# Performance work log

Hardware: AMD Instinct MI355X
Metric: run time of the kernel (lower is better)

The kernel has to match this reference:

```python
import jax, jax.numpy as jnp
import numpy as np

N_NODES = 50000
N_EDGES = 800000
D_IN = 128
D_HID = 128
BN_EPS = 1e-5


def _sage_mean(h, src, dst, w_self, w_neigh, b):
    # DGL SAGEConv('mean'): out = h @ W_self + mean_{neighbors}(h_src) @ W_neigh + bias
    msg = h[src]                                               # [E, D] gather
    ssum = jax.ops.segment_sum(msg, dst, num_segments=N_NODES)  # [N, D]
    deg = jax.ops.segment_sum(jnp.ones((src.shape[0],), h.dtype), dst,
                              num_segments=N_NODES)            # [N]
    mean = ssum / jnp.maximum(deg, 1.0)[:, None]
    return h @ w_self + mean @ w_neigh + b


def _bn_relu(h, gamma, beta):
    # BatchNorm1d with batch statistics (training-mode math), then ReLU.
    m = jnp.mean(h, axis=0)
    v = jnp.mean(jnp.square(h - m), axis=0)  # biased variance, as torch uses for normalization
    hn = (h - m) * jax.lax.rsqrt(v + BN_EPS) * gamma + beta
    return jax.nn.relu(hn)


def setup_inputs() -> dict:
    key = jax.random.key(0)
    ks = jax.random.split(key, 16)
    x = jax.random.normal(ks[0], (N_NODES, D_IN), dtype=jnp.float32)
    src = jax.random.randint(ks[1], (N_EDGES,), 0, N_NODES, dtype=jnp.int32)
    dst = jax.random.randint(ks[2], (N_EDGES,), 0, N_NODES, dtype=jnp.int32)
    s0 = 1.0 / np.sqrt(D_IN)
    s1 = 1.0 / np.sqrt(D_HID)
    inp = {
        'x': x, 'src': src, 'dst': dst,
        'W_self0': jax.random.uniform(ks[3], (D_IN, D_HID), jnp.float32, -s0, s0),
        'W_neigh0': jax.random.uniform(ks[4], (D_IN, D_HID), jnp.float32, -s0, s0),
        'b0': jnp.zeros((D_HID,), jnp.float32),
        'W_self1': jax.random.uniform(ks[5], (D_HID, D_HID), jnp.float32, -s1, s1),
        'W_neigh1': jax.random.uniform(ks[6], (D_HID, D_HID), jnp.float32, -s1, s1),
        'b1': jnp.zeros((D_HID,), jnp.float32),
        'W_self2': jax.random.uniform(ks[7], (D_HID, D_HID), jnp.float32, -s1, s1),
        'W_neigh2': jax.random.uniform(ks[8], (D_HID, D_HID), jnp.float32, -s1, s1),
        'b2': jnp.zeros((D_HID,), jnp.float32),
        'gamma0': jnp.ones((D_HID,), jnp.float32),
        'beta0': jnp.zeros((D_HID,), jnp.float32),
        'gamma1': jnp.ones((D_HID,), jnp.float32),
        'beta1': jnp.zeros((D_HID,), jnp.float32),
    }
    return inp


def reference(x, src, dst,
              W_self0, W_neigh0, b0,
              W_self1, W_neigh1, b1,
              W_self2, W_neigh2, b2,
              gamma0, beta0, gamma1, beta1):
    h = _sage_mean(x, src, dst, W_self0, W_neigh0, b0)
    h = _bn_relu(h, gamma0, beta0)  # dropout is identity in eval mode
    h = _sage_mean(h, src, dst, W_self1, W_neigh1, b1)
    h = _bn_relu(h, gamma1, beta1)
    h = _sage_mean(h, src, dst, W_self2, W_neigh2, b2)
    return h
```

## Files before the change

### kernel.cpp

```cpp
#include <hip/hip_runtime.h>

#define N_NODES 50000
#define N_EDGES 800000
#define D 128
#define BN_EPS 1e-5f

#define NBUCK 391
#define BSHIFT 7
#define S1_BLOCKS 256
#define EPB 3125
#define CVT_BLOCKS 6250
#define PACK_BLOCKS 384
#define NREP 16
#define NSLICE 8
#define SSHIFT 13
#define BN_BLOCKS 512

typedef __attribute__((ext_vector_type(8))) short bf16x8;
typedef __attribute__((ext_vector_type(4))) float f32x4;
typedef __attribute__((ext_vector_type(2))) float f32x2;

__device__ inline unsigned short f2bf(float f) {
    unsigned int u = __float_as_uint(f);
    u = (u + 0x7FFF + ((u >> 16) & 1)) >> 16;
    return (unsigned short)u;
}

__device__ inline float bf2f(unsigned short b) {
    return __uint_as_float(((unsigned)b) << 16);
}

__device__ __forceinline__ void acc_plain(f32x2* a, uint4 v) {
    unsigned w[4] = {v.x, v.y, v.z, v.w};
#pragma unroll
    for (int p = 0; p < 4; p++) {
        f32x2 f;
        f.x = __uint_as_float(w[p] << 16);
        f.y = __uint_as_float(w[p] & 0xffff0000u);
        a[p] += f;
    }
}


__global__ void fused_prep(const float* __restrict__ x, unsigned short* __restrict__ x16,
                           const int* __restrict__ dst, int* __restrict__ hist,
                           const float* __restrict__ Ws0, const float* __restrict__ Wn0,
                           const float* __restrict__ Ws1, const float* __restrict__ Wn1,
                           const float* __restrict__ Ws2, const float* __restrict__ Wn2,
                           unsigned short* __restrict__ Wf, float* __restrict__ statsg) {
    __shared__ int lh[NBUCK];
    const int bid = blockIdx.x, t = threadIdx.x;

    if (bid < CVT_BLOCKS) {
        int idx = bid * 256 + t;
        float4 v = ((const float4*)x)[idx];
        ushort4 o;
        o.x = f2bf(v.x); o.y = f2bf(v.y); o.z = f2bf(v.z); o.w = f2bf(v.w);
        ((ushort4*)x16)[idx] = o;
    } else if (bid < CVT_BLOCKS + S1_BLOCKS) {
        int blk = bid - CVT_BLOCKS;
        for (int i = t; i < NBUCK; i += 256) lh[i] = 0;
        __syncthreads();
        int e0 = blk * EPB;
        for (int i = 0; i < 13; i++) {
            int k = t + i * 256;
            if (k < EPB) atomicAdd(&lh[dst[e0 + k] >> BSHIFT], 1);
        }
        __syncthreads();
        for (int i = t; i < NBUCK; i += 256) hist[blk * NBUCK + i] = lh[i];
    } else {
        if (bid == CVT_BLOCKS + S1_BLOCKS) {
            for (int i = t; i < 2 * NREP * 256; i += 256) statsg[i] = 0.f;
        }
        int idx = (bid - (CVT_BLOCKS + S1_BLOCKS)) * 256 + t;
        if (idx < 3 * 32768) {
            int layer = idx >> 15;
            int rem = idx & 32767;
            int kt = rem >> 12;
            int nt = (rem >> 9) & 7;
            int lane = (rem >> 3) & 63;
            int j = rem & 7;
            int k = kt * 32 + (lane >> 4) * 8 + j;
            int n = nt * 16 + (lane & 15);
            const float* Wsrc;
            if (layer == 0) Wsrc = (k < 128) ? Ws0 : Wn0;
            else if (layer == 1) Wsrc = (k < 128) ? Ws1 : Wn1;
            else Wsrc = (k < 128) ? Ws2 : Wn2;
            Wf[idx] = f2bf(Wsrc[(k & 127) * D + n]);
        }
    }
}


__global__ void s2a(int* __restrict__ hist, int* __restrict__ bucketTotal) {
    __shared__ int s[S1_BLOCKS];
    int b = blockIdx.x, t = threadIdx.x;
    int v = hist[t * NBUCK + b];
    s[t] = v;
    __syncthreads();
    for (int off = 1; off < S1_BLOCKS; off <<= 1) {
        int x = (t >= off) ? s[t - off] : 0;
        __syncthreads();
        s[t] += x;
        __syncthreads();
    }
    hist[t * NBUCK + b] = s[t] - v;
    if (t == S1_BLOCKS - 1) bucketTotal[b] = s[t];
}


__global__ void s3_scatter(const int* __restrict__ src, const int* __restrict__ dst,
                           const int* __restrict__ hist, const int* __restrict__ bucketTotal,
                           int* __restrict__ bucketStart, unsigned int* __restrict__ rec) {
    __shared__ int sc[512];
    __shared__ int base[NBUCK];
    int blk = blockIdx.x, t = threadIdx.x;
    int i1 = t + 256;
    int v0 = (t < NBUCK) ? bucketTotal[t] : 0;
    int v1 = (i1 < NBUCK) ? bucketTotal[i1] : 0;
    sc[t] = v0; sc[i1] = v1;
    __syncthreads();
    for (int off = 1; off < 512; off <<= 1) {
        int x0 = (t >= off) ? sc[t - off] : 0;
        int x1 = (i1 >= off) ? sc[i1 - off] : 0;
        __syncthreads();
        sc[t] += x0; sc[i1] += x1;
        __syncthreads();
    }
    if (t < NBUCK)  base[t]  = (sc[t] - v0)  + hist[blk * NBUCK + t];
    if (i1 < NBUCK) base[i1] = (sc[i1] - v1) + hist[blk * NBUCK + i1];
    if (blk == 0) {
        if (t < NBUCK)  bucketStart[t]  = sc[t] - v0;
        if (i1 < NBUCK) bucketStart[i1] = sc[i1] - v1;
        if (t == 0) bucketStart[NBUCK] = N_EDGES;
    }
    __syncthreads();
    int e0 = blk * EPB;
    for (int i = 0; i < 13; i++) {
        int k = t + i * 256;
        if (k < EPB) {
            int e = e0 + k;
            int d = dst[e];
            int p = atomicAdd(&base[d >> BSHIFT], 1);
            rec[p] = ((unsigned)(d & 127) << 16) | (unsigned)src[e];
        }
    }
}


__global__ void s4_build(const unsigned int* __restrict__ rec, const int* __restrict__ bucketStart,
                         unsigned short* __restrict__ csr, int* __restrict__ degi,
                         int* __restrict__ offsets, float* __restrict__ inv_deg) {
    __shared__ int cnt[128 * NSLICE];
    __shared__ int exc[128 * NSLICE];
    __shared__ int lcur[128 * NSLICE];
    __shared__ int ls[256];
    int b = blockIdx.x, t = threadIdx.x;
    int start = bucketStart[b], end = bucketStart[b + 1];

    for (int i = t; i < 128 * NSLICE; i += 256) cnt[i] = 0;
    __syncthreads();
    for (int e = start + t; e < end; e += 256) {
        unsigned r = rec[e];
        int key = ((r >> 16) << 3) | ((r & 0xFFFFu) >> SSHIFT);
        atomicAdd(&cnt[key], 1);
    }
    __syncthreads();

    int c0 = cnt[4 * t], c1 = cnt[4 * t + 1], c2 = cnt[4 * t + 2], c3 = cnt[4 * t + 3];
    int sum4 = c0 + c1 + c2 + c3;
    ls[t] = sum4;
    __syncthreads();
    for (int off = 1; off < 256; off <<= 1) {
        int x = (t >= off) ? ls[t - off] : 0;
        __syncthreads();
        ls[t] += x;
        __syncthreads();
    }
    int base = ls[t] - sum4;
    exc[4 * t]     = base;
    exc[4 * t + 1] = base + c0;
    exc[4 * t + 2] = base + c0 + c1;
    exc[4 * t + 3] = base + c0 + c1 + c2;
    lcur[4 * t]     = start + base;
    lcur[4 * t + 1] = start + base + c0;
    lcur[4 * t + 2] = start + base + c0 + c1;
    lcur[4 * t + 3] = start + base + c0 + c1 + c2;
    __syncthreads();

    if (t < 128) {
        int node = (b << BSHIFT) + t;
        int e0 = exc[8 * t];
        int e1 = (t == 127) ? (end - start) : exc[8 * t + 8];
        int v = e1 - e0;
        if (node < N_NODES) {
            degi[node] = v;
            offsets[node] = start + e0;
            inv_deg[node] = 1.0f / (float)max(v, 1);
        }
    }
    __syncthreads();
    for (int e = start + t; e < end; e += 256) {
        unsigned r = rec[e];
        int key = ((r >> 16) << 3) | ((r & 0xFFFFu) >> SSHIFT);
        int p = atomicAdd(&lcur[key], 1);
        csr[p] = (unsigned short)(r & 0xFFFFu);
    }
}


__global__ void bn_relu_apply(unsigned short* __restrict__ h,
                              const float* __restrict__ stats,
                              const float* __restrict__ gamma, const float* __restrict__ beta) {
    __shared__ float sc[128], sh[128];
    int t = threadIdx.x;
    if (t < 128) {
        const float invN = 1.0f / (float)N_NODES;
        float s = 0.f, q = 0.f;
#pragma unroll
        for (int r = 0; r < NREP; r++) {
            s += stats[r * 256 + t];
            q += stats[r * 256 + 128 + t];
        }
        float m = s * invN;
        float var = q * invN - m * m;
        float scv = rsqrtf(var + BN_EPS) * gamma[t];
        sc[t] = scv;
        sh[t] = beta[t] - m * scv;
    }
    __syncthreads();
    const int total = N_NODES * D / 8;
    for (int idx = blockIdx.x * 256 + t; idx < total; idx += BN_BLOCKS * 256) {
        uint4 v = ((const uint4*)h)[idx];
        int col0 = (idx & 15) * 8;
        unsigned w[4] = {v.x, v.y, v.z, v.w};
        unsigned ow[4];
#pragma unroll
        for (int p = 0; p < 4; p++) {
            float lo = __uint_as_float(w[p] << 16);
            float hi = __uint_as_float(w[p] & 0xffff0000u);
            float rlo = fmaxf(lo * sc[col0 + 2 * p]     + sh[col0 + 2 * p],     0.f);
            float rhi = fmaxf(hi * sc[col0 + 2 * p + 1] + sh[col0 + 2 * p + 1], 0.f);
            ow[p] = ((unsigned)f2bf(rhi) << 16) | f2bf(rlo);
        }
        uint4 o;
        o.x = ow[0]; o.y = ow[1]; o.z = ow[2]; o.w = ow[3];
        ((uint4*)h)[idx] = o;
    }
}


#define GROW(r) (*(const uint4*)(hb + ((size_t)(r) << 7)))
#define ROWIDX(k) __shfl((int)((k) < 16 ? cb0 : ((k) < 32 ? cb1 : cb2)), (k) & 15, 16)

__global__ void aggregate16(const unsigned short* __restrict__ h16,
                            const unsigned short* __restrict__ csr, const int* __restrict__ offsets,
                            const int* __restrict__ degi, const float* __restrict__ inv_deg,
                            unsigned short* __restrict__ mean16) {
    int t = threadIdx.x;
    int node = blockIdx.x * 16 + (t >> 4);
    int c = t & 15;
    const unsigned short* hb = h16 + c * 8;
    int beg = offsets[node], n = degi[node];

    int ci = beg + c;
    int cmax = N_EDGES - 1;
    unsigned cb0 = csr[min(ci, cmax)];
    unsigned cb1 = csr[min(ci + 16, cmax)];
    unsigned cb2 = csr[min(ci + 32, cmax)];

    f32x2 a[4];
#pragma unroll
    for (int j = 0; j < 4; j++) a[j] = (f32x2)(0.f);

    int nfast = n < 48 ? n : 48;
    int i = 0;
    if (nfast >= 4) {
        uint4 v0 = GROW(ROWIDX(0)), v1 = GROW(ROWIDX(1));
        uint4 v2 = GROW(ROWIDX(2)), v3 = GROW(ROWIDX(3));
        for (i = 4; i + 3 < nfast; i += 4) {
            int r0 = ROWIDX(i), r1 = ROWIDX(i + 1), r2 = ROWIDX(i + 2), r3 = ROWIDX(i + 3);
            uint4 w0 = GROW(r0), w1 = GROW(r1), w2 = GROW(r2), w3 = GROW(r3);
            acc_plain(a, v0); acc_plain(a, v1); acc_plain(a, v2); acc_plain(a, v3);
            v0 = w0; v1 = w1; v2 = w2; v3 = w3;
        }
        acc_plain(a, v0); acc_plain(a, v1); acc_plain(a, v2); acc_plain(a, v3);
    }
    for (; i < nfast; i++) { uint4 v = GROW(ROWIDX(i)); acc_plain(a, v); }
    for (; i < n; i++) { int r = csr[beg + i]; uint4 v = GROW(r); acc_plain(a, v); }

    float w = inv_deg[node];
    uint4 o;
    o.x = ((unsigned)f2bf(a[0].y * w) << 16) | f2bf(a[0].x * w);
    o.y = ((unsigned)f2bf(a[1].y * w) << 16) | f2bf(a[1].x * w);
    o.z = ((unsigned)f2bf(a[2].y * w) << 16) | f2bf(a[2].x * w);
    o.w = ((unsigned)f2bf(a[3].y * w) << 16) | f2bf(a[3].x * w);
    *(uint4*)(mean16 + (size_t)node * D + c * 8) = o;
}


__global__ __launch_bounds__(256, 4) void sage_gemm(
    const unsigned short* __restrict__ h16, const unsigned short* __restrict__ mean16,
    const unsigned short* __restrict__ Wf, const float* __restrict__ bias,
    unsigned short* __restrict__ out16, float* __restrict__ outf,
    float* __restrict__ statsOut) {
    __shared__ unsigned short sWf[16384];
    __shared__ float sstat[256];
    const int t = threadIdx.x;
    const int lane = t & 63;
    const int m = lane & 15;
    const int quad = lane >> 4;
    const int wrow0 = blockIdx.x * 64 + (t >> 6) * 16;

    int arow = wrow0 + m;
    if (arow >= N_NODES) arow = N_NODES - 1;

    bf16x8 afr[8];
#pragma unroll
    for (int kt = 0; kt < 4; kt++)
        afr[kt] = *(const bf16x8*)(h16 + (size_t)arow * D + kt * 32 + quad * 8);
#pragma unroll
    for (int kt = 0; kt < 4; kt++)
        afr[4 + kt] = *(const bf16x8*)(mean16 + (size_t)arow * D + kt * 32 + quad * 8);

    const uint4* W4 = (const uint4*)Wf;
    uint4* S4 = (uint4*)sWf;
#pragma unroll
    for (int i = 0; i < 8; i++) S4[i * 256 + t] = W4[i * 256 + t];
    if (statsOut) sstat[t] = 0.f;
    __syncthreads();

    f32x4 acc[8];
#pragma unroll
    for (int i = 0; i < 8; i++) acc[i] = (f32x4)(0.f);

#pragma unroll
    for (int kt = 0; kt < 4; kt++) {
#pragma unroll
        for (int nt = 0; nt < 8; nt++) {
            bf16x8 bf = *(const bf16x8*)(sWf + ((kt * 8 + nt) * 64 + lane) * 8);
            acc[nt] = __builtin_amdgcn_mfma_f32_16x16x32_bf16(afr[kt], bf, acc[nt], 0, 0, 0);
        }
    }

    __syncthreads();
#pragma unroll
    for (int i = 0; i < 8; i++) S4[i * 256 + t] = W4[2048 + i * 256 + t];
    __syncthreads();

#pragma unroll
    for (int kt = 4; kt < 8; kt++) {
#pragma unroll
        for (int nt = 0; nt < 8; nt++) {
            bf16x8 bf = *(const bf16x8*)(sWf + (((kt - 4) * 8 + nt) * 64 + lane) * 8);
            acc[nt] = __builtin_amdgcn_mfma_f32_16x16x32_bf16(afr[kt], bf, acc[nt], 0, 0, 0);
        }
    }

    const bool do16 = (out16 != nullptr);
#pragma unroll
    for (int nt = 0; nt < 8; nt++) {
        int cidx = nt * 16 + m;
        float bv = bias[cidx];
        float s = 0.f, q = 0.f;
#pragma unroll
        for (int reg = 0; reg < 4; reg++) {
            int r = wrow0 + quad * 4 + reg;
            float v = acc[nt][reg] + bv;
            if (r < N_NODES) {
                if (do16) out16[(size_t)r * D + cidx] = f2bf(v);
                else      outf[(size_t)r * D + cidx] = v;
                s += v; q += v * v;
            }
        }
        if (statsOut) {
            s += __shfl_xor(s, 16); s += __shfl_xor(s, 32);
            q += __shfl_xor(q, 16); q += __shfl_xor(q, 32);
            if (quad == 0) {
                atomicAdd(&sstat[cidx], s);
                atomicAdd(&sstat[128 + cidx], q);
            }
        }
    }
    if (statsOut) {
        __syncthreads();
        atomicAdd(&statsOut[(blockIdx.x & (NREP - 1)) * 256 + t], sstat[t]);
    }
}


extern "C" void kernel_launch(void* const* d_in, const int* in_sizes, int n_in,
                              void* d_out, int out_size, void* d_ws, size_t ws_size,
                              hipStream_t stream) {
    const float* x   = (const float*)d_in[0];
    const int* src   = (const int*)d_in[1];
    const int* dst   = (const int*)d_in[2];
    const float* Ws0 = (const float*)d_in[3];
    const float* Wn0 = (const float*)d_in[4];
    const float* b0  = (const float*)d_in[5];
    const float* Ws1 = (const float*)d_in[6];
    const float* Wn1 = (const float*)d_in[7];
    const float* b1  = (const float*)d_in[8];
    const float* Ws2 = (const float*)d_in[9];
    const float* Wn2 = (const float*)d_in[10];
    const float* b2  = (const float*)d_in[11];
    const float* g0  = (const float*)d_in[12];
    const float* be0 = (const float*)d_in[13];
    const float* g1  = (const float*)d_in[14];
    const float* be1 = (const float*)d_in[15];

    char* base = (char*)d_ws;
    size_t NND = (size_t)N_NODES * D;
    unsigned short* X16    = (unsigned short*)base;
    unsigned short* H16    = (unsigned short*)(base + NND * 2);
    unsigned short* mean16 = (unsigned short*)(base + 2 * NND * 2);
    char* p = base + 6 * NND;
    unsigned short* Wf = (unsigned short*)p;  p += 3 * 32768 * 2;
    int* hist          = (int*)p;             p += (size_t)S1_BLOCKS * NBUCK * 4;
    int* bucketTotal   = (int*)p;             p += 1568;
    int* bucketStart   = (int*)p;             p += 1600;
    unsigned int* rec  = (unsigned int*)p;    p += (size_t)N_EDGES * 4;
    unsigned short* csr = (unsigned short*)p; p += (size_t)N_EDGES * 2;
    int* degi    = (int*)p;                   p += N_NODES * 4;
    int* offsets = (int*)p;                   p += N_NODES * 4;
    float* inv_deg = (float*)p;               p += N_NODES * 4;
    float* stats   = (float*)p;               p += 2 * NREP * 256 * 4;
    float* stats0 = stats, *stats1 = stats + NREP * 256;

    fused_prep<<<CVT_BLOCKS + S1_BLOCKS + PACK_BLOCKS, 256, 0, stream>>>(
        x, X16, dst, hist, Ws0, Wn0, Ws1, Wn1, Ws2, Wn2, Wf, stats);
    s2a<<<NBUCK, 256, 0, stream>>>(hist, bucketTotal);
    s3_scatter<<<S1_BLOCKS, 256, 0, stream>>>(src, dst, hist, bucketTotal, bucketStart, rec);
    s4_build<<<NBUCK, 256, 0, stream>>>(rec, bucketStart, csr, degi, offsets, inv_deg);

    const int AGG_B = (N_NODES + 15) / 16;
    const int GEMM_B = (N_NODES + 63) / 64;

    aggregate16<<<AGG_B, 256, 0, stream>>>(X16, csr, offsets, degi, inv_deg, mean16);
    sage_gemm<<<GEMM_B, 256, 0, stream>>>(X16, mean16, Wf, b0, H16, nullptr, stats0);

    bn_relu_apply<<<BN_BLOCKS, 256, 0, stream>>>(H16, stats0, g0, be0);
    aggregate16<<<AGG_B, 256, 0, stream>>>(H16, csr, offsets, degi, inv_deg, mean16);
    sage_gemm<<<GEMM_B, 256, 0, stream>>>(H16, mean16, Wf + 32768, b1, X16, nullptr, stats1);

    bn_relu_apply<<<BN_BLOCKS, 256, 0, stream>>>(X16, stats1, g1, be1);
    aggregate16<<<AGG_B, 256, 0, stream>>>(X16, csr, offsets, degi, inv_deg, mean16);
    sage_gemm<<<GEMM_B, 256, 0, stream>>>(X16, mean16, Wf + 65536, b2, nullptr,
                                          (float*)d_out, nullptr);
}
```

Measured before the change: 278.0 us.

## Fuse neighbor-mean aggregation into SAGE GEMM via swizzled shared memory

Merges the separate aggregate kernel into the GEMM kernel: each 64-row block first gathers and averages neighbor rows for its own nodes into a swizzled shared-memory tile, then reads the mean fragments from LDS for the MFMA. This removes the global mean16 round trip and three kernel launches per forward. Weight staging is cut to quarter-size chunks to make room for the mean tile, which adds more barriers and loses the parallelism of the 16-node aggregate blocks, since each block now runs four aggregation passes serially.

```diff
diff --git a/kernel.cpp b/kernel.cpp
--- a/kernel.cpp
+++ b/kernel.cpp
@@ -253,58 +253,15 @@
 #define GROW(r) (*(const uint4*)(hb + ((size_t)(r) << 7)))
 #define ROWIDX(k) __shfl((int)((k) < 16 ? cb0 : ((k) < 32 ? cb1 : cb2)), (k) & 15, 16)
 
-__global__ void aggregate16(const unsigned short* __restrict__ h16,
-                            const unsigned short* __restrict__ csr, const int* __restrict__ offsets,
-                            const int* __restrict__ degi, const float* __restrict__ inv_deg,
-                            unsigned short* __restrict__ mean16) {
-    int t = threadIdx.x;
-    int node = blockIdx.x * 16 + (t >> 4);
-    int c = t & 15;
-    const unsigned short* hb = h16 + c * 8;
-    int beg = offsets[node], n = degi[node];
-
-    int ci = beg + c;
-    int cmax = N_EDGES - 1;
-    unsigned cb0 = csr[min(ci, cmax)];
-    unsigned cb1 = csr[min(ci + 16, cmax)];
-    unsigned cb2 = csr[min(ci + 32, cmax)];
-
-    f32x2 a[4];
-#pragma unroll
-    for (int j = 0; j < 4; j++) a[j] = (f32x2)(0.f);
-
-    int nfast = n < 48 ? n : 48;
-    int i = 0;
-    if (nfast >= 4) {
-        uint4 v0 = GROW(ROWIDX(0)), v1 = GROW(ROWIDX(1));
-        uint4 v2 = GROW(ROWIDX(2)), v3 = GROW(ROWIDX(3));
-        for (i = 4; i + 3 < nfast; i += 4) {
-            int r0 = ROWIDX(i), r1 = ROWIDX(i + 1), r2 = ROWIDX(i + 2), r3 = ROWIDX(i + 3);
-            uint4 w0 = GROW(r0), w1 = GROW(r1), w2 = GROW(r2), w3 = GROW(r3);
-            acc_plain(a, v0); acc_plain(a, v1); acc_plain(a, v2); acc_plain(a, v3);
-            v0 = w0; v1 = w1; v2 = w2; v3 = w3;
-        }
-        acc_plain(a, v0); acc_plain(a, v1); acc_plain(a, v2); acc_plain(a, v3);
-    }
-    for (; i < nfast; i++) { uint4 v = GROW(ROWIDX(i)); acc_plain(a, v); }
-    for (; i < n; i++) { int r = csr[beg + i]; uint4 v = GROW(r); acc_plain(a, v); }
-
-    float w = inv_deg[node];
-    uint4 o;
-    o.x = ((unsigned)f2bf(a[0].y * w) << 16) | f2bf(a[0].x * w);
-    o.y = ((unsigned)f2bf(a[1].y * w) << 16) | f2bf(a[1].x * w);
-    o.z = ((unsigned)f2bf(a[2].y * w) << 16) | f2bf(a[2].x * w);
-    o.w = ((unsigned)f2bf(a[3].y * w) << 16) | f2bf(a[3].x * w);
-    *(uint4*)(mean16 + (size_t)node * D + c * 8) = o;
-}
-
-
-__global__ __launch_bounds__(256, 4) void sage_gemm(
-    const unsigned short* __restrict__ h16, const unsigned short* __restrict__ mean16,
+__global__ __launch_bounds__(256, 4) void agg_gemm(
+    const unsigned short* __restrict__ h16,
+    const unsigned short* __restrict__ csr, const int* __restrict__ offsets,
+    const int* __restrict__ degi, const float* __restrict__ inv_deg,
     const unsigned short* __restrict__ Wf, const float* __restrict__ bias,
     unsigned short* __restrict__ out16, float* __restrict__ outf,
     float* __restrict__ statsOut) {
-    __shared__ unsigned short sWf[16384];
+    __shared__ unsigned short sWf[8192];
+    __shared__ unsigned short smean[8192];
     __shared__ float sstat[256];
     const int t = threadIdx.x;
     const int lane = t & 63;
@@ -319,41 +276,82 @@
 #pragma unroll
     for (int kt = 0; kt < 4; kt++)
         afr[kt] = *(const bf16x8*)(h16 + (size_t)arow * D + kt * 32 + quad * 8);
-#pragma unroll
-    for (int kt = 0; kt < 4; kt++)
-        afr[4 + kt] = *(const bf16x8*)(mean16 + (size_t)arow * D + kt * 32 + quad * 8);
+
+    if (statsOut) sstat[t] = 0.f;
+
+    int c = t & 15;
+    const unsigned short* hb = h16 + c * 8;
+    const int cmax = N_EDGES - 1;
+#pragma unroll 1
+    for (int it = 0; it < 4; it++) {
+        int local = it * 16 + (t >> 4);
+        int node = blockIdx.x * 64 + local;
+        int valid = node < N_NODES;
+        int beg = valid ? offsets[node] : 0;
+        int n = valid ? degi[node] : 0;
+
+        int ci = beg + c;
+        unsigned cb0 = csr[min(ci, cmax)];
+        unsigned cb1 = csr[min(ci + 16, cmax)];
+        unsigned cb2 = csr[min(ci + 32, cmax)];
+
+        f32x2 a[4];
+#pragma unroll
+        for (int j = 0; j < 4; j++) a[j] = (f32x2)(0.f);
+
+        int nfast = n < 48 ? n : 48;
+        int i = 0;
+        if (nfast >= 4) {
+            uint4 v0 = GROW(ROWIDX(0)), v1 = GROW(ROWIDX(1));
+            uint4 v2 = GROW(ROWIDX(2)), v3 = GROW(ROWIDX(3));
+            for (i = 4; i + 3 < nfast; i += 4) {
+                int r0 = ROWIDX(i), r1 = ROWIDX(i + 1), r2 = ROWIDX(i + 2), r3 = ROWIDX(i + 3);
+                uint4 w0 = GROW(r0), w1 = GROW(r1), w2 = GROW(r2), w3 = GROW(r3);
+                acc_plain(a, v0); acc_plain(a, v1); acc_plain(a, v2); acc_plain(a, v3);
+                v0 = w0; v1 = w1; v2 = w2; v3 = w3;
+            }
+            acc_plain(a, v0); acc_plain(a, v1); acc_plain(a, v2); acc_plain(a, v3);
+        }
+        for (; i < nfast; i++) { uint4 v = GROW(ROWIDX(i)); acc_plain(a, v); }
+        for (; i < n; i++) { int r = csr[beg + i]; uint4 v = GROW(r); acc_plain(a, v); }
+
+        float w = valid ? inv_deg[node] : 0.f;
+        uint4 o;
+        o.x = ((unsigned)f2bf(a[0].y * w) << 16) | f2bf(a[0].x * w);
+        o.y = ((unsigned)f2bf(a[1].y * w) << 16) | f2bf(a[1].x * w);
+        o.z = ((unsigned)f2bf(a[2].y * w) << 16) | f2bf(a[2].x * w);
+        o.w = ((unsigned)f2bf(a[3].y * w) << 16) | f2bf(a[3].x * w);
+        unsigned off = (unsigned)(local * 256 + c * 16) ^ (unsigned)((local & 7) << 4);
+        *(uint4*)((char*)smean + off) = o;
+    }
+    __syncthreads();
+
+#pragma unroll
+    for (int kt = 0; kt < 4; kt++) {
+        unsigned off = (unsigned)(((t >> 6) * 16 + m) * 256 + kt * 64 + quad * 16)
+                     ^ (unsigned)((m & 7) << 4);
+        afr[4 + kt] = *(const bf16x8*)((const char*)smean + off);
+    }
+
+    f32x4 acc[8];
+#pragma unroll
+    for (int i = 0; i < 8; i++) acc[i] = (f32x4)(0.f);
 
     const uint4* W4 = (const uint4*)Wf;
     uint4* S4 = (uint4*)sWf;
-#pragma unroll
-    for (int i = 0; i < 8; i++) S4[i * 256 + t] = W4[i * 256 + t];
-    if (statsOut) sstat[t] = 0.f;
-    __syncthreads();
-
-    f32x4 acc[8];
-#pragma unroll
-    for (int i = 0; i < 8; i++) acc[i] = (f32x4)(0.f);
-
-#pragma unroll
-    for (int kt = 0; kt < 4; kt++) {
-#pragma unroll
-        for (int nt = 0; nt < 8; nt++) {
-            bf16x8 bf = *(const bf16x8*)(sWf + ((kt * 8 + nt) * 64 + lane) * 8);
-            acc[nt] = __builtin_amdgcn_mfma_f32_16x16x32_bf16(afr[kt], bf, acc[nt], 0, 0, 0);
-        }
-    }
-
-    __syncthreads();
-#pragma unroll
-    for (int i = 0; i < 8; i++) S4[i * 256 + t] = W4[2048 + i * 256 + t];
-    __syncthreads();
-
-#pragma unroll
-    for (int kt = 4; kt < 8; kt++) {
-#pragma unroll
-        for (int nt = 0; nt < 8; nt++) {
-            bf16x8 bf = *(const bf16x8*)(sWf + (((kt - 4) * 8 + nt) * 64 + lane) * 8);
-            acc[nt] = __builtin_amdgcn_mfma_f32_16x16x32_bf16(afr[kt], bf, acc[nt], 0, 0, 0);
+#pragma unroll 1
+    for (int q = 0; q < 4; q++) {
+        if (q) __syncthreads();
+#pragma unroll
+        for (int i = 0; i < 4; i++) S4[i * 256 + t] = W4[q * 1024 + i * 256 + t];
+        __syncthreads();
+#pragma unroll
+        for (int kk = 0; kk < 2; kk++) {
+#pragma unroll
+            for (int nt = 0; nt < 8; nt++) {
+                bf16x8 bf = *(const bf16x8*)(sWf + ((kk * 8 + nt) * 64 + lane) * 8);
+                acc[nt] = __builtin_amdgcn_mfma_f32_16x16x32_bf16(afr[q * 2 + kk], bf, acc[nt], 0, 0, 0);
+            }
         }
     }
 
@@ -413,8 +411,7 @@
     size_t NND = (size_t)N_NODES * D;
     unsigned short* X16    = (unsigned short*)base;
     unsigned short* H16    = (unsigned short*)(base + NND * 2);
-    unsigned short* mean16 = (unsigned short*)(base + 2 * NND * 2);
-    char* p = base + 6 * NND;
+    char* p = base + 4 * NND;
     unsigned short* Wf = (unsigned short*)p;  p += 3 * 32768 * 2;
     int* hist          = (int*)p;             p += (size_t)S1_BLOCKS * NBUCK * 4;
     int* bucketTotal   = (int*)p;             p += 1568;
@@ -433,18 +430,16 @@
     s3_scatter<<<S1_BLOCKS, 256, 0, stream>>>(src, dst, hist, bucketTotal, bucketStart, rec);
     s4_build<<<NBUCK, 256, 0, stream>>>(rec, bucketStart, csr, degi, offsets, inv_deg);
 
-    const int AGG_B = (N_NODES + 15) / 16;
     const int GEMM_B = (N_NODES + 63) / 64;
 
-    aggregate16<<<AGG_B, 256, 0, stream>>>(X16, csr, offsets, degi, inv_deg, mean16);
-    sage_gemm<<<GEMM_B, 256, 0, stream>>>(X16, mean16, Wf, b0, H16, nullptr, stats0);
+    agg_gemm<<<GEMM_B, 256, 0, stream>>>(X16, csr, offsets, degi, inv_deg,
+                                         Wf, b0, H16, nullptr, stats0);
 
     bn_relu_apply<<<BN_BLOCKS, 256, 0, stream>>>(H16, stats0, g0, be0);
-    aggregate16<<<AGG_B, 256, 0, stream>>>(H16, csr, offsets, degi, inv_deg, mean16);
-    sage_gemm<<<GEMM_B, 256, 0, stream>>>(H16, mean16, Wf + 32768, b1, X16, nullptr, stats1);
+    agg_gemm<<<GEMM_B, 256, 0, stream>>>(H16, csr, offsets, degi, inv_deg,
+                                         Wf + 32768, b1, X16, nullptr, stats1);
 
     bn_relu_apply<<<BN_BLOCKS, 256, 0, stream>>>(X16, stats1, g1, be1);
-    aggregate16<<<AGG_B, 256, 0, stream>>>(X16, csr, offsets, degi, inv_deg, mean16);
-    sage_gemm<<<GEMM_B, 256, 0, stream>>>(X16, mean16, Wf + 65536, b2, nullptr,
-                                          (float*)d_out, nullptr);
-}
+    agg_gemm<<<GEMM_B, 256, 0, stream>>>(X16, csr, offsets, degi, inv_deg,
+                                         Wf + 65536, b2, nullptr, (float*)d_out, nullptr);
+}
```

After: 293.0 us. +5.4%, slower.
